# Optimization experiments

Hardware: AMD Instinct MI355X
Metric: run time of the kernel (lower is better)

Reference implementation:

```python
import jax, jax.numpy as jnp
import numpy as np

EPS = 1e-6
H = 12  # num_attention_heads

def _phi(x):
    # feature map used by fast-transformers LinearAttention: elu(x) + 1
    return jax.nn.elu(x) + 1.0

def setup_inputs() -> dict:
    key = jax.random.key(0)
    k1, k2, k3 = jax.random.split(key, 3)
    B, N, D = 32, 1024, 768
    x = jax.random.normal(k1, (B, N, D), dtype=jnp.float32)
    W_qkv = jax.random.normal(k2, (D, 3 * D), dtype=jnp.float32) * (D ** -0.5)
    W_out = jax.random.normal(k3, (D, D), dtype=jnp.float32) * (D ** -0.5)
    b_out = jnp.zeros((D,), dtype=jnp.float32)
    return {"x": x, "W_qkv": W_qkv, "W_out": W_out, "b_out": b_out}

def reference(x, W_qkv, W_out, b_out):
    B, N, D = x.shape
    d = D // H
    # F.pad(x, [0,0,0,1]): append one zero token along sequence
    x_ = jnp.pad(x, ((0, 0), (0, 1), (0, 0)))              # [B, N+1, D]
    qkv = x_ @ W_qkv                                        # [B, N+1, 3D]
    q, k, v = jnp.split(qkv, 3, axis=-1)
    q = q.reshape(B, N + 1, H, d)
    k = k.reshape(B, N + 1, H, d)
    v = v.reshape(B, N + 1, H, d)
    # non-causal linear attention (mask is all-ones -> no masking)
    q = _phi(q)
    k = _phi(k)
    kv = jnp.einsum('bshd,bshm->bhdm', k, v)                # [B, H, d, d]
    z = 1.0 / (jnp.einsum('blhd,bhd->blh', q, k.sum(axis=1)) + EPS)
    out = jnp.einsum('blhd,bhdm,blh->blhm', q, kv, z)       # [B, N+1, H, d]
    out = out.reshape(B, N + 1, D)
    out = out @ W_out + b_out                               # dropout = identity (eval)
    return out[:, :-1, :]                                   # drop padding token
```

## Files before the change

kernel.cpp:

```cpp
#include <hip/hip_runtime.h>
#include <hip/hip_bf16.h>


typedef __bf16 bf16x8 __attribute__((ext_vector_type(8)));
typedef float f32x4 __attribute__((ext_vector_type(4)));

__device__ __forceinline__ ushort f2bf(float f) {
  union { float f; unsigned u; } x; x.f = f;
  unsigned r = x.u + 0x7fffu + ((x.u >> 16) & 1u);
  return (ushort)(r >> 16);
}
__device__ __forceinline__ float bf2f(ushort h) {
  union { unsigned u; float f; } x; x.u = ((unsigned)h) << 16;
  return x.f;
}
__device__ __forceinline__ float bits2f(unsigned u) {
  union { unsigned u; float f; } x; x.u = u;
  return x.f;
}
__device__ __forceinline__ void gload_lds16(const void* g, void* lds) {
  __builtin_amdgcn_global_load_lds((const __attribute__((address_space(1))) void*)g,
                                   (__attribute__((address_space(3))) void*)lds, 16, 0, 0);
}

__global__ __launch_bounds__(256) void cvt_f32_bf16(const float* __restrict__ in,
                                                    ushort* __restrict__ out, int n4) {
  int i = blockIdx.x * 256 + threadIdx.x;
  if (i >= n4) return;
  float4 v = reinterpret_cast<const float4*>(in)[i];
  ushort4 o;
  o.x = f2bf(v.x); o.y = f2bf(v.y); o.z = f2bf(v.z); o.w = f2bf(v.w);
  reinterpret_cast<ushort4*>(out)[i] = o;
}

__global__ __launch_bounds__(256) void transpose_cvt(const float* __restrict__ src,
                                                     ushort* __restrict__ dst, int R, int C) {
  __shared__ float tile[32][33];
  int bc = blockIdx.x * 32, br = blockIdx.y * 32;
  int tx = threadIdx.x & 31, ty = threadIdx.x >> 5;
  #pragma unroll
  for (int i = 0; i < 32; i += 8)
    tile[ty + i][tx] = src[(size_t)(br + ty + i) * C + (bc + tx)];
  __syncthreads();
  #pragma unroll
  for (int i = 0; i < 32; i += 8)
    dst[(size_t)(bc + ty + i) * R + (br + tx)] = f2bf(tile[tx][ty + i]);
}

template <int MODE>
__global__ __launch_bounds__(256) void gemm128(const ushort* __restrict__ A,
                                               const ushort* __restrict__ Bt,
                                               void* __restrict__ C,
                                               const float* __restrict__ bias,
                                               int N, int K, int nbx, int cpx) {
  __shared__ ushort As[128 * 32];
  __shared__ ushort Bs[128 * 32];
  const int tid = threadIdx.x;
  const int lane = tid & 63;
  const int wid = tid >> 6;
  const int wm = wid >> 1, wn = wid & 1;
  const int laneR = lane & 15, laneS = lane >> 4;

  const int bid = blockIdx.x;
  const int lin = (bid & 7) * cpx + (bid >> 3);
  const int by = lin / nbx, bx = lin - by * nbx;
  const int m0 = by * 128, n0 = bx * 128;
  const int NT = K >> 5;

  const int srow0 = tid >> 2, dslot = tid & 3;
  const int sslot = dslot ^ ((srow0 >> 1) & 3);
  const ushort* Asrc = A + (size_t)(m0 + srow0) * K + sslot * 8;
  const ushort* Bsrc = Bt + (size_t)(n0 + srow0) * K + sslot * 8;
  const size_t rowstep64 = (size_t)64 * K;
  const int ldst = tid * 8;

  const int sprime = laneS ^ ((laneR >> 1) & 3);
  const int aoff = (wm * 64 + laneR) * 32 + sprime * 8;
  const int boff = (wn * 64 + laneR) * 32 + sprime * 8;

  f32x4 acc[4][4] = {};

  for (int kt = 0; kt < NT; ++kt) {
    const int kb = kt * 32;
    __syncthreads();
    gload_lds16(Asrc + kb,             As + ldst);
    gload_lds16(Asrc + kb + rowstep64, As + 2048 + ldst);
    gload_lds16(Bsrc + kb,             Bs + ldst);
    gload_lds16(Bsrc + kb + rowstep64, Bs + 2048 + ldst);
    asm volatile("s_waitcnt vmcnt(0)" ::: "memory");
    __syncthreads();
    bf16x8 a[4], b[4];
    #pragma unroll
    for (int i = 0; i < 4; ++i) {
      a[i] = *reinterpret_cast<const bf16x8*>(&As[aoff + i * 512]);
      b[i] = *reinterpret_cast<const bf16x8*>(&Bs[boff + i * 512]);
    }
    #pragma unroll
    for (int i = 0; i < 4; ++i)
      #pragma unroll
      for (int j = 0; j < 4; ++j)
        acc[i][j] = __builtin_amdgcn_mfma_f32_16x16x32_bf16(a[i], b[j], acc[i][j], 0, 0, 0);
  }

  #pragma unroll
  for (int i = 0; i < 4; ++i) {
    const int grow0 = m0 + wm * 64 + i * 16 + (laneS << 2);
    #pragma unroll
    for (int j = 0; j < 4; ++j) {
      const int gcol = n0 + wn * 64 + j * 16 + laneR;
      #pragma unroll
      for (int r = 0; r < 4; ++r) {
        float v = acc[i][j][r];
        if (MODE == 0) {
          if (gcol < 1536) v = (v > 0.f) ? (v + 1.f) : __expf(v);
          reinterpret_cast<ushort*>(C)[(size_t)(grow0 + r) * N + gcol] = f2bf(v);
        } else {
          reinterpret_cast<float*>(C)[(size_t)(grow0 + r) * N + gcol] = v + bias[gcol];
        }
      }
    }
  }
}

__global__ __launch_bounds__(256) void kv_partial(const ushort* __restrict__ qkv,
                                                  float* __restrict__ kv_part,
                                                  float* __restrict__ ks_part) {
  const int blk = blockIdx.x;
  const int bh = blk >> 2, sp = blk & 3;
  const int b = bh / 12, h = bh % 12;
  const int tid = threadIdx.x;
  __shared__ float Ks[32 * 64];
  __shared__ float Vs[32 * 64];
  float acc[4][4] = {};
  float kacc[4] = {};
  const int dq0 = (tid & 15) * 4, mq0 = (tid >> 4) * 4;
  const int r = tid >> 3, o = (tid & 7) * 8;
  for (int st = 0; st < 256; st += 32) {
    const size_t rowbase = (size_t)(b * 1024 + sp * 256 + st + r) * 2304 + h * 64 + o;
    int4 kraw = *reinterpret_cast<const int4*>(qkv + rowbase + 768);
    int4 vraw = *reinterpret_cast<const int4*>(qkv + rowbase + 1536);
    float kf[8], vf[8];
    {
      const unsigned* kw = reinterpret_cast<const unsigned*>(&kraw);
      const unsigned* vw = reinterpret_cast<const unsigned*>(&vraw);
      #pragma unroll
      for (int w = 0; w < 4; ++w) {
        kf[2 * w]     = bits2f(kw[w] << 16);
        kf[2 * w + 1] = bits2f(kw[w] & 0xffff0000u);
        vf[2 * w]     = bits2f(vw[w] << 16);
        vf[2 * w + 1] = bits2f(vw[w] & 0xffff0000u);
      }
    }
    __syncthreads();
    #pragma unroll
    for (int w = 0; w < 8; ++w) {
      Ks[r * 64 + o + w] = kf[w];
      Vs[r * 64 + o + w] = vf[w];
    }
    __syncthreads();
    #pragma unroll 8
    for (int s = 0; s < 32; ++s) {
      f32x4 kk = *reinterpret_cast<const f32x4*>(&Ks[s * 64 + dq0]);
      f32x4 vv = *reinterpret_cast<const f32x4*>(&Vs[s * 64 + mq0]);
      #pragma unroll
      for (int jm = 0; jm < 4; ++jm)
        #pragma unroll
        for (int id = 0; id < 4; ++id)
          acc[jm][id] += vv[jm] * kk[id];
      if (mq0 == 0) {
        #pragma unroll
        for (int id = 0; id < 4; ++id) kacc[id] += kk[id];
      }
    }
  }
  float* kvp = kv_part + ((size_t)sp * 384 + bh) * 4096;
  #pragma unroll
  for (int jm = 0; jm < 4; ++jm)
    #pragma unroll
    for (int id = 0; id < 4; ++id)
      kvp[(mq0 + jm) * 64 + dq0 + id] = acc[jm][id];
  if (mq0 == 0) {
    #pragma unroll
    for (int id = 0; id < 4; ++id)
      ks_part[((size_t)sp * 384 + bh) * 64 + dq0 + id] = kacc[id];
  }
}

__global__ __launch_bounds__(256) void kv_reduce(const float* __restrict__ kv_part,
                                                 const float* __restrict__ ks_part,
                                                 ushort* __restrict__ kv_bf,
                                                 float* __restrict__ ksum) {
  int i = blockIdx.x * 256 + threadIdx.x;
  if (i < 384 * 4096) {
    float s = 0.f;
    #pragma unroll
    for (int p = 0; p < 4; ++p) s += kv_part[(size_t)p * (384 * 4096) + i];
    kv_bf[i] = f2bf(s);
  }
  if (i < 384 * 64) {
    float s = 1.0f;
    #pragma unroll
    for (int p = 0; p < 4; ++p) s += ks_part[(size_t)p * (384 * 64) + i];
    ksum[i] = s;
  }
}

__global__ __launch_bounds__(256) void attn_kernel(const ushort* __restrict__ qkv,
                                                   const ushort* __restrict__ kv_bf,
                                                   const float* __restrict__ ksum,
                                                   ushort* __restrict__ attn) {
  const int blk = blockIdx.x;
  const int bh = blk >> 3, tb = blk & 7;
  const int b = bh / 12, h = bh % 12;
  const int row0 = b * 1024 + tb * 128;
  __shared__ ushort Qs[128 * 64];
  __shared__ ushort KVs[64 * 64];
  __shared__ float zs[128];
  __shared__ float ks_lds[64];
  const int tid = threadIdx.x;
  const int lane = tid & 63, w = tid >> 6;
  #pragma unroll
  for (int j = 0; j < 4; ++j) {
    int c = j * 256 + tid;
    gload_lds16(qkv + (size_t)(row0 + (c >> 3)) * 2304 + h * 64 + (c & 7) * 8, &Qs[c * 8]);
  }
  #pragma unroll
  for (int j = 0; j < 2; ++j) {
    int c = j * 256 + tid;
    gload_lds16(kv_bf + (size_t)bh * 4096 + c * 8, &KVs[c * 8]);
  }
  if (tid < 64) ks_lds[tid] = ksum[bh * 64 + tid];
  asm volatile("s_waitcnt vmcnt(0)" ::: "memory");
  __syncthreads();
  if (tid < 128) {
    float d = 0.f;
    #pragma unroll 8
    for (int e = 0; e < 64; ++e) d += bf2f(Qs[tid * 64 + e]) * ks_lds[e];
    zs[tid] = 1.f / (d + 1e-6f);
  }
  __syncthreads();
  f32x4 acc[2][4] = {};
  #pragma unroll
  for (int ks = 0; ks < 2; ++ks) {
    bf16x8 a[2], bb[4];
    #pragma unroll
    for (int i = 0; i < 2; ++i)
      a[i] = *reinterpret_cast<const bf16x8*>(&Qs[(w * 32 + i * 16 + (lane & 15)) * 64 + ks * 32 + (lane >> 4) * 8]);
    #pragma unroll
    for (int j = 0; j < 4; ++j)
      bb[j] = *reinterpret_cast<const bf16x8*>(&KVs[(j * 16 + (lane & 15)) * 64 + ks * 32 + (lane >> 4) * 8]);
    #pragma unroll
    for (int i = 0; i < 2; ++i)
      #pragma unroll
      for (int j = 0; j < 4; ++j)
        acc[i][j] = __builtin_amdgcn_mfma_f32_16x16x32_bf16(a[i], bb[j], acc[i][j], 0, 0, 0);
  }
  #pragma unroll
  for (int i = 0; i < 2; ++i) {
    const int t0 = w * 32 + i * 16 + ((lane >> 4) << 2);
    #pragma unroll
    for (int j = 0; j < 4; ++j) {
      const int m = j * 16 + (lane & 15);
      #pragma unroll
      for (int r = 0; r < 4; ++r) {
        float v = acc[i][j][r] * zs[t0 + r];
        attn[(size_t)(row0 + t0 + r) * 768 + h * 64 + m] = f2bf(v);
      }
    }
  }
}

extern "C" void kernel_launch(void* const* d_in, const int* in_sizes, int n_in,
                              void* d_out, int out_size, void* d_ws, size_t ws_size,
                              hipStream_t stream) {
  (void)in_sizes; (void)n_in; (void)out_size; (void)ws_size;
  const float* x    = (const float*)d_in[0];
  const float* Wqkv = (const float*)d_in[1];
  const float* Wout = (const float*)d_in[2];
  const float* bout = (const float*)d_in[3];
  float* out = (float*)d_out;
  char* ws = (char*)d_ws;

  ushort* xbf    = (ushort*)(ws);
  ushort* wqkvT  = (ushort*)(ws + 50331648);
  ushort* woutT  = (ushort*)(ws + 53870592);
  ushort* qkv    = (ushort*)(ws + 55050240);
  float*  ksp    = (float*) (ws + 206045184);
  ushort* kvbf   = (ushort*)(ws + 206438400);
  float*  ksum   = (float*) (ws + 209584128);
  float*  kvpart = (float*)(ws);
  ushort* attn   = (ushort*)(ws);

  cvt_f32_bf16<<<24576, 256, 0, stream>>>(x, xbf, 6291456);
  transpose_cvt<<<dim3(72, 24), 256, 0, stream>>>(Wqkv, wqkvT, 768, 2304);
  transpose_cvt<<<dim3(24, 24), 256, 0, stream>>>(Wout, woutT, 768, 768);
  gemm128<0><<<4608, 256, 0, stream>>>(xbf, wqkvT, qkv, nullptr, 2304, 768, 18, 576);
  kv_partial<<<1536, 256, 0, stream>>>(qkv, kvpart, ksp);
  kv_reduce<<<6144, 256, 0, stream>>>(kvpart, ksp, kvbf, ksum);
  attn_kernel<<<3072, 256, 0, stream>>>(qkv, kvbf, ksum, attn);
  gemm128<1><<<1536, 256, 0, stream>>>(attn, woutT, out, bout, 768, 768, 6, 192);
}
```

Measured before the change: 341.6 us.

## Triple-buffer GEMM with 128x256 tiles and swizzle LDS in attention kernels

Replaces the single-buffered 128x128 GEMM with a 512-thread, 128x256-tile kernel that uses a three-stage LDS ring, so global-to-LDS loads for later K-tiles overlap the MFMA work, with raised wave priority around the MFMA block. It also pads the kv_partial LDS rows to reduce bank conflicts. The attention kernel now XOR-swizzles its Q and KV LDS layout and reads Q with vector loads in the normalizer loop. The risks are higher LDS use per block (72 KB of dynamic shared memory) and more barriers per iteration.

After: 290.4 us. 15.0% less time.

```diff
diff --git a/kernel.cpp b/kernel.cpp
--- a/kernel.cpp
+++ b/kernel.cpp
@@ -48,59 +48,78 @@
 }
 
 template <int MODE>
-__global__ __launch_bounds__(256) void gemm128(const ushort* __restrict__ A,
-                                               const ushort* __restrict__ Bt,
-                                               void* __restrict__ C,
-                                               const float* __restrict__ bias,
-                                               int N, int K, int nbx, int cpx) {
-  __shared__ ushort As[128 * 32];
-  __shared__ ushort Bs[128 * 32];
+__global__ __launch_bounds__(512, 4) void gemm3b(const ushort* __restrict__ A,
+                                                 const ushort* __restrict__ Bt,
+                                                 void* __restrict__ C,
+                                                 const float* __restrict__ bias,
+                                                 int N, int K, int nbx, int cpx) {
+  extern __shared__ ushort lds[];
   const int tid = threadIdx.x;
   const int lane = tid & 63;
   const int wid = tid >> 6;
-  const int wm = wid >> 1, wn = wid & 1;
+  const int wm = wid >> 2, wn = wid & 3;
   const int laneR = lane & 15, laneS = lane >> 4;
 
   const int bid = blockIdx.x;
   const int lin = (bid & 7) * cpx + (bid >> 3);
   const int by = lin / nbx, bx = lin - by * nbx;
-  const int m0 = by * 128, n0 = bx * 128;
+  const int m0 = by * 128, n0 = bx * 256;
   const int NT = K >> 5;
 
-  const int srow0 = tid >> 2, dslot = tid & 3;
-  const int sslot = dslot ^ ((srow0 >> 1) & 3);
-  const ushort* Asrc = A + (size_t)(m0 + srow0) * K + sslot * 8;
-  const ushort* Bsrc = Bt + (size_t)(n0 + srow0) * K + sslot * 8;
-  const size_t rowstep64 = (size_t)64 * K;
-  const int ldst = tid * 8;
+  const int sr = tid >> 2, ss = tid & 3;
+  const int sslot = ss ^ ((sr >> 1) & 3);
+  const ushort* Asrc = A + (size_t)(m0 + sr) * K + sslot * 8;
+  const ushort* Bsrc = Bt + (size_t)(n0 + sr) * K + sslot * 8;
+  const size_t rowstep128 = (size_t)128 * K;
+  const int ldstA = tid * 8;
+  const int ldstB = 4096 + tid * 8;
 
   const int sprime = laneS ^ ((laneR >> 1) & 3);
   const int aoff = (wm * 64 + laneR) * 32 + sprime * 8;
-  const int boff = (wn * 64 + laneR) * 32 + sprime * 8;
+  const int boff = 4096 + (wn * 64 + laneR) * 32 + sprime * 8;
 
   f32x4 acc[4][4] = {};
 
-  for (int kt = 0; kt < NT; ++kt) {
-    const int kb = kt * 32;
-    __syncthreads();
-    gload_lds16(Asrc + kb,             As + ldst);
-    gload_lds16(Asrc + kb + rowstep64, As + 2048 + ldst);
-    gload_lds16(Bsrc + kb,             Bs + ldst);
-    gload_lds16(Bsrc + kb + rowstep64, Bs + 2048 + ldst);
-    asm volatile("s_waitcnt vmcnt(0)" ::: "memory");
-    __syncthreads();
+  #define SBAR  __builtin_amdgcn_sched_barrier(0)
+  #define STAGE_T(KT, DB)                                                         \
+    { gload_lds16(Asrc + (KT) * 32, lds + (DB) + ldstA);                          \
+      gload_lds16(Bsrc + (KT) * 32, lds + (DB) + ldstB);                          \
+      gload_lds16(Bsrc + (KT) * 32 + rowstep128, lds + (DB) + ldstB + 4096); }
+
+  STAGE_T(0, 0);
+  STAGE_T(1, 12288);
+  asm volatile("s_waitcnt vmcnt(3)" ::: "memory");
+  SBAR;
+  __builtin_amdgcn_s_barrier();
+  SBAR;
+
+  for (int t = 0; t < NT; ++t) {
+    const ushort* cb = lds + (t % 3) * 12288;
+    const int db2 = ((t + 2) % 3) * 12288;
+    const int t2 = (t + 2 < NT) ? t + 2 : t;
     bf16x8 a[4], b[4];
     #pragma unroll
-    for (int i = 0; i < 4; ++i) {
-      a[i] = *reinterpret_cast<const bf16x8*>(&As[aoff + i * 512]);
-      b[i] = *reinterpret_cast<const bf16x8*>(&Bs[boff + i * 512]);
-    }
+    for (int j = 0; j < 4; ++j) b[j] = *(const bf16x8*)(cb + boff + j * 512);
+    #pragma unroll
+    for (int i = 0; i < 4; ++i) a[i] = *(const bf16x8*)(cb + aoff + i * 512);
+    STAGE_T(t2, db2);
+    asm volatile("s_waitcnt vmcnt(3)" ::: "memory");
+    SBAR;
+    __builtin_amdgcn_s_barrier();
+    SBAR;
+    __builtin_amdgcn_s_setprio(1);
     #pragma unroll
     for (int i = 0; i < 4; ++i)
       #pragma unroll
       for (int j = 0; j < 4; ++j)
         acc[i][j] = __builtin_amdgcn_mfma_f32_16x16x32_bf16(a[i], b[j], acc[i][j], 0, 0, 0);
-  }
+    __builtin_amdgcn_s_setprio(0);
+    SBAR;
+    __builtin_amdgcn_s_barrier();
+    SBAR;
+  }
+  #undef STAGE_T
+  asm volatile("s_waitcnt vmcnt(0)" ::: "memory");
 
   #pragma unroll
   for (int i = 0; i < 4; ++i) {
@@ -129,8 +148,8 @@
   const int bh = blk >> 2, sp = blk & 3;
   const int b = bh / 12, h = bh % 12;
   const int tid = threadIdx.x;
-  __shared__ float Ks[32 * 64];
-  __shared__ float Vs[32 * 64];
+  __shared__ float Ks[32 * 68];
+  __shared__ float Vs[32 * 68];
   float acc[4][4] = {};
   float kacc[4] = {};
   const int dq0 = (tid & 15) * 4, mq0 = (tid >> 4) * 4;
@@ -154,14 +173,14 @@
     __syncthreads();
     #pragma unroll
     for (int w = 0; w < 8; ++w) {
-      Ks[r * 64 + o + w] = kf[w];
-      Vs[r * 64 + o + w] = vf[w];
+      Ks[r * 68 + o + w] = kf[w];
+      Vs[r * 68 + o + w] = vf[w];
     }
     __syncthreads();
     #pragma unroll 8
     for (int s = 0; s < 32; ++s) {
-      f32x4 kk = *reinterpret_cast<const f32x4*>(&Ks[s * 64 + dq0]);
-      f32x4 vv = *reinterpret_cast<const f32x4*>(&Vs[s * 64 + mq0]);
+      f32x4 kk = *reinterpret_cast<const f32x4*>(&Ks[s * 68 + dq0]);
+      f32x4 vv = *reinterpret_cast<const f32x4*>(&Vs[s * 68 + mq0]);
       #pragma unroll
       for (int jm = 0; jm < 4; ++jm)
         #pragma unroll
@@ -222,33 +241,48 @@
   #pragma unroll
   for (int j = 0; j < 4; ++j) {
     int c = j * 256 + tid;
-    gload_lds16(qkv + (size_t)(row0 + (c >> 3)) * 2304 + h * 64 + (c & 7) * 8, &Qs[c * 8]);
+    int qr = c >> 3, dsl = c & 7;
+    int ssl = dsl ^ (qr & 7);
+    gload_lds16(qkv + (size_t)(row0 + qr) * 2304 + h * 64 + ssl * 8, &Qs[c * 8]);
   }
   #pragma unroll
   for (int j = 0; j < 2; ++j) {
     int c = j * 256 + tid;
-    gload_lds16(kv_bf + (size_t)bh * 4096 + c * 8, &KVs[c * 8]);
+    int mr = c >> 3, dsl = c & 7;
+    int ssl = dsl ^ (mr & 7);
+    gload_lds16(kv_bf + (size_t)bh * 4096 + mr * 64 + ssl * 8, &KVs[c * 8]);
   }
   if (tid < 64) ks_lds[tid] = ksum[bh * 64 + tid];
   asm volatile("s_waitcnt vmcnt(0)" ::: "memory");
   __syncthreads();
   if (tid < 128) {
     float d = 0.f;
-    #pragma unroll 8
-    for (int e = 0; e < 64; ++e) d += bf2f(Qs[tid * 64 + e]) * ks_lds[e];
+    const int tx7 = tid & 7;
+    #pragma unroll
+    for (int s = 0; s < 8; ++s) {
+      int4 raw = *reinterpret_cast<const int4*>(&Qs[tid * 64 + ((s ^ tx7) << 3)]);
+      const unsigned* wds = reinterpret_cast<const unsigned*>(&raw);
+      #pragma unroll
+      for (int w2 = 0; w2 < 4; ++w2) {
+        d += bits2f(wds[w2] << 16) * ks_lds[s * 8 + 2 * w2];
+        d += bits2f(wds[w2] & 0xffff0000u) * ks_lds[s * 8 + 2 * w2 + 1];
+      }
+    }
     zs[tid] = 1.f / (d + 1e-6f);
   }
   __syncthreads();
   f32x4 acc[2][4] = {};
+  const int lr7 = (lane & 15) & 7;
   #pragma unroll
   for (int ks = 0; ks < 2; ++ks) {
+    const int sxor = ((ks * 4 + (lane >> 4)) ^ lr7) << 3;
     bf16x8 a[2], bb[4];
     #pragma unroll
     for (int i = 0; i < 2; ++i)
-      a[i] = *reinterpret_cast<const bf16x8*>(&Qs[(w * 32 + i * 16 + (lane & 15)) * 64 + ks * 32 + (lane >> 4) * 8]);
+      a[i] = *reinterpret_cast<const bf16x8*>(&Qs[(w * 32 + i * 16 + (lane & 15)) * 64 + sxor]);
     #pragma unroll
     for (int j = 0; j < 4; ++j)
-      bb[j] = *reinterpret_cast<const bf16x8*>(&KVs[(j * 16 + (lane & 15)) * 64 + ks * 32 + (lane >> 4) * 8]);
+      bb[j] = *reinterpret_cast<const bf16x8*>(&KVs[(j * 16 + (lane & 15)) * 64 + sxor]);
     #pragma unroll
     for (int i = 0; i < 2; ++i)
       #pragma unroll
@@ -291,12 +325,18 @@
   float*  kvpart = (float*)(ws);
   ushort* attn   = (ushort*)(ws);
 
+  static const int LDS3 = 73728;
+  hipFuncSetAttribute(reinterpret_cast<const void*>(&gemm3b<0>),
+                      hipFuncAttributeMaxDynamicSharedMemorySize, LDS3);
+  hipFuncSetAttribute(reinterpret_cast<const void*>(&gemm3b<1>),
+                      hipFuncAttributeMaxDynamicSharedMemorySize, LDS3);
+
   cvt_f32_bf16<<<24576, 256, 0, stream>>>(x, xbf, 6291456);
   transpose_cvt<<<dim3(72, 24), 256, 0, stream>>>(Wqkv, wqkvT, 768, 2304);
   transpose_cvt<<<dim3(24, 24), 256, 0, stream>>>(Wout, woutT, 768, 768);
-  gemm128<0><<<4608, 256, 0, stream>>>(xbf, wqkvT, qkv, nullptr, 2304, 768, 18, 576);
+  gemm3b<0><<<2304, 512, LDS3, stream>>>(xbf, wqkvT, qkv, nullptr, 2304, 768, 9, 288);
   kv_partial<<<1536, 256, 0, stream>>>(qkv, kvpart, ksp);
   kv_reduce<<<6144, 256, 0, stream>>>(kvpart, ksp, kvbf, ksum);
   attn_kernel<<<3072, 256, 0, stream>>>(qkv, kvbf, ksum, attn);
-  gemm128<1><<<1536, 256, 0, stream>>>(attn, woutT, out, bout, 768, 768, 6, 192);
-}
+  gemm3b<1><<<768, 512, LDS3, stream>>>(attn, woutT, out, bout, 768, 768, 3, 96);
+}
```
